# Kernel optimization log

Measured on AMD Instinct MI355X. Metric: run time of the kernel, lower is better.

## Reference

```python
import jax, jax.numpy as jnp
import numpy as np

IN_F = 4096
OUT_F = 11008
P8 = 128
P6 = 256
P4 = IN_F - P8 - P6  # 3712


def setup_inputs() -> dict:
    key = jax.random.key(0)
    k1, k2, k3, k4 = jax.random.split(key, 4)
    x = jax.random.normal(k1, (32, 8, IN_F), dtype=jnp.float32)
    W = jax.random.normal(k2, (OUT_F, IN_F), dtype=jnp.float32) * 0.02
    bias = jax.random.normal(k3, (OUT_F,), dtype=jnp.float32) * 0.01
    # channel permutation: first P4 channels -> 4-bit, next P6 -> 6-bit, last P8 -> 8-bit outliers
    reorder_index = jax.random.permutation(k4, IN_F).astype(jnp.int32)
    return {"x": x, "W": W, "bias": bias, "reorder_index": reorder_index}


def _quant(v, bits):
    # symmetric per-row quantization (per-token for acts, per-out-channel for weights)
    qmax = float(2 ** (bits - 1) - 1)
    s = jnp.max(jnp.abs(v), axis=-1, keepdims=True) / qmax
    s = jnp.where(s == 0, jnp.ones_like(s), s)
    q = jnp.round(jnp.clip(v / s, -qmax, qmax))
    return q, s


def reference(x, W, bias, reorder_index):
    bsz, q_len, F = x.shape
    xr = x.reshape(bsz * q_len, F)[:, reorder_index]  # reorder_quantize_x gather
    Wr = W[:, reorder_index]                          # reorder_quantize_w4 gather
    y = jnp.zeros((bsz * q_len, W.shape[0]), dtype=x.dtype)
    start = 0
    for bits, n in ((4, P4), (6, P6), (8, P8)):
        qa, sa = _quant(xr[:, start:start + n], bits)      # [T,n], [T,1]
        qb, sb = _quant(Wr[:, start:start + n], bits)      # [O,n], [O,1]
        # dequantized partial matmul: (qa @ qb.T) * sa * sb.T
        y = y + jnp.einsum('tn,on->to', qa, qb) * (sa * sb.T)
        start += n
    y = y + bias
    return y.reshape(bsz, q_len, -1)
```

## Files before the change

kernel.cpp:

```cpp
#include <hip/hip_runtime.h>
#include <stdint.h>

#define T_ROWS 256
#define KF 4096
#define OF 11008
#define WROW 2240

typedef int   v4i __attribute__((ext_vector_type(4)));
typedef float v4f __attribute__((ext_vector_type(4)));
typedef unsigned int u32;

typedef const __attribute__((address_space(1))) uint8_t* gptr_t;
typedef __attribute__((address_space(3))) uint8_t* lptr_t;

__global__ __launch_bounds__(256) void perm_k(const int* __restrict__ idx,
                                              int* __restrict__ src_of) {
    __shared__ uint8_t g[KF];
    __shared__ int cnt[3][256];
    __shared__ int exc[3][256];
    const int t = threadIdx.x;
    for (int i = 0; i < 16; ++i) {
        int p = t * 16 + i;
        int seg = p < 3712 ? 0 : (p < 3968 ? 1 : 2);
        g[idx[p]] = (uint8_t)seg;
    }
    __syncthreads();
    int c0 = 0, c1 = 0, c2 = 0;
    for (int i = 0; i < 16; ++i) {
        int s = g[t * 16 + i];
        c0 += (s == 0); c1 += (s == 1); c2 += (s == 2);
    }
    cnt[0][t] = c0; cnt[1][t] = c1; cnt[2][t] = c2;
    __syncthreads();
    if (t < 192) {
        int s = t >> 6, l = t & 63;
        int run = 0;
        for (int j = 0; j < 4; ++j) {
            int x = cnt[s][j * 64 + l];
            int inc = x;
#pragma unroll
            for (int off = 1; off < 64; off <<= 1) {
                int y = __shfl_up(inc, off);
                if (l >= off) inc += y;
            }
            exc[s][j * 64 + l] = run + inc - x;
            run += __shfl(inc, 63);
        }
    }
    __syncthreads();
    int off0 = exc[0][t], off1 = 3712 + exc[1][t], off2 = 3968 + exc[2][t];
    for (int i = 0; i < 16; ++i) {
        int c = t * 16 + i;
        int s = g[c];
        int d = (s == 0) ? off0++ : (s == 1) ? off1++ : off2++;
        src_of[d] = c;
    }
}

__global__ __launch_bounds__(256) void quant_k(const float* __restrict__ x,
                                               const float* __restrict__ W,
                                               const int* __restrict__ src_of,
                                               int8_t* __restrict__ qX,
                                               uint8_t* __restrict__ qWp,
                                               float* __restrict__ sX,
                                               float* __restrict__ sW,
                                               int* __restrict__ S0X) {
    __shared__ float rowbuf[KF];
    __shared__ float lmax[256];
    __shared__ float sm[3];
    __shared__ int isum[256];
    const int b = blockIdx.x;
    const int t = threadIdx.x;
    const int w = t >> 6, lane = t & 63;
    const bool isX = b < T_ROWS;
    const int r = isX ? b : b - T_ROWS;
    const float* row = (isX ? x : W) + (size_t)r * KF;

#pragma unroll
    for (int j = 0; j < 4; ++j) {
        const uint8_t* src = (const uint8_t*)(row + j * 1024 + t * 4);
        __builtin_amdgcn_global_load_lds((gptr_t)src, (lptr_t)&rowbuf[j * 1024 + w * 256], 16, 0, 0);
    }

    const int seg = t < 232 ? 0 : (t < 248 ? 1 : 2);
    const float qmax = seg == 0 ? 7.f : (seg == 1 ? 31.f : 127.f);
    int c[16];
#pragma unroll
    for (int i = 0; i < 4; ++i) {
        v4i ci = *(const v4i*)&src_of[t * 16 + i * 4];
        c[i*4+0] = ci[0]; c[i*4+1] = ci[1]; c[i*4+2] = ci[2]; c[i*4+3] = ci[3];
    }
    __syncthreads();

    float v[16];
    float mx = 0.f;
#pragma unroll
    for (int i = 0; i < 16; ++i) { v[i] = rowbuf[c[i]]; mx = fmaxf(mx, fabsf(v[i])); }
    lmax[t] = mx;
    __syncthreads();
    if (w == 0) {
        float m = fmaxf(fmaxf(lmax[lane], lmax[lane + 64]), lmax[lane + 128]);
        if (lane < 40) m = fmaxf(m, lmax[lane + 192]);
#pragma unroll
        for (int off = 32; off; off >>= 1) m = fmaxf(m, __shfl_xor(m, off));
        if (lane == 0) sm[0] = m;
    } else if (w == 1) {
        float m = lane < 16 ? lmax[232 + lane] : 0.f;
#pragma unroll
        for (int off = 8; off; off >>= 1) m = fmaxf(m, __shfl_xor(m, off));
        if (lane == 0) sm[1] = m;
    } else if (w == 2) {
        float m = lane < 8 ? lmax[248 + lane] : 0.f;
#pragma unroll
        for (int off = 4; off; off >>= 1) m = fmaxf(m, __shfl_xor(m, off));
        if (lane == 0) sm[2] = m;
    }
    __syncthreads();
    float s = sm[seg] / qmax;
    if (s == 0.f) s = 1.f;
    if (t == 0 || t == 232 || t == 248)
        (isX ? sX : sW)[seg * (isX ? T_ROWS : OF) + r] = s;

    int q[16];
#pragma unroll
    for (int i = 0; i < 16; ++i)
        q[i] = (int)rintf(fminf(fmaxf(v[i] / s, -qmax), qmax));

    if (isX) {
        int ss = 0;
        union { int8_t bb[16]; v4i vv; } u;
#pragma unroll
        for (int i = 0; i < 16; ++i) { u.bb[i] = (int8_t)q[i]; ss += q[i]; }
        isum[t] = (seg == 0) ? ss : 0;
        *(v4i*)(qX + (size_t)r * KF + t * 16) = u.vv;
        __syncthreads();
        if (w == 0) {
            int v2 = isum[lane] + isum[lane + 64] + isum[lane + 128] + isum[lane + 192];
#pragma unroll
            for (int off = 32; off; off >>= 1) v2 += __shfl_xor(v2, off);
            if (lane == 0) S0X[r] = v2;
        }
    } else {
        uint8_t* wrow = qWp + (size_t)r * WROW;
        if (seg == 0) {
            u32 pk[2] = {0, 0};
#pragma unroll
            for (int j = 0; j < 8; ++j) {
                u32 byte = (u32)(q[2*j] + 8) | ((u32)(q[2*j+1] + 8) << 4);
                pk[j >> 2] |= byte << ((j & 3) * 8);
            }
            *(u32*)(wrow + t * 8) = pk[0];
            *(u32*)(wrow + t * 8 + 4) = pk[1];
        } else {
            union { int8_t bb[16]; v4i vv; } u;
#pragma unroll
            for (int i = 0; i < 16; ++i) u.bb[i] = (int8_t)q[i];
            const int off = (seg == 1) ? 1856 + (t - 232) * 16 : 2112 + (t - 248) * 16;
            *(v4i*)(wrow + off) = u.vv;
        }
    }
}

__global__ __launch_bounds__(256, 2)
void gemm_k(const int8_t* __restrict__ qX, const uint8_t* __restrict__ qWp,
            const float* __restrict__ sX, const float* __restrict__ sW,
            const int* __restrict__ S0X,
            const float* __restrict__ bias, float* __restrict__ out) {
    __shared__ __align__(16) int8_t lA[3][128 * 128];
    __shared__ __align__(16) int8_t lB[2][64 * 128];

    const int bid = blockIdx.x;
    const int swz = (bid & 7) * 43 + (bid >> 3);
    const int mb = swz & 1;
    const int nb = swz >> 1;
    const int row0 = mb * 128;
    const int col0 = nb * 64;
    const int tid = threadIdx.x;
    const int lane = tid & 63;
    const int w = tid >> 6;
    const int lr = lane >> 3, lc = lane & 7;
    const int brow = tid >> 2;
    const int bch  = tid & 3;

    v4i iacc[2][4];
    v4f facc[2][4];
#pragma unroll
    for (int m = 0; m < 2; ++m)
#pragma unroll
        for (int n = 0; n < 4; ++n) {
            iacc[m][n][0]=0; iacc[m][n][1]=0; iacc[m][n][2]=0; iacc[m][n][3]=0;
            facc[m][n][0]=0.f; facc[m][n][1]=0.f; facc[m][n][2]=0.f; facc[m][n][3]=0.f;
        }

    auto stageA = [&](int slot, int step) {
        const int k0 = step * 128;
        const int sc = (lc ^ lr) << 4;
#pragma unroll
        for (int j = 0; j < 4; ++j) {
            const int row = j * 32 + w * 8;
            const uint8_t* src = (const uint8_t*)qX + (size_t)(row0 + row + lr) * KF + k0 + sc;
            __builtin_amdgcn_global_load_lds((gptr_t)src, (lptr_t)&lA[slot][row * 128], 16, 0, 0);
        }
    };

    auto loadB = [&](v4i (&rs)[2], int step) {
        const uint8_t* rb = qWp + (size_t)(col0 + brow) * WROW;
        if (step <= 28) {
            rs[0] = *(const v4i*)(rb + step * 64 + bch * 16);
        } else {
            const int off = step * 128 - 1856;
            rs[0] = *(const v4i*)(rb + off + bch * 32);
            rs[1] = *(const v4i*)(rb + off + bch * 32 + 16);
        }
    };

    auto writeB = [&](v4i (&rs)[2], int step) {
        int8_t* dst = &lB[step & 1][0];
        const int swr = brow & 7;
        v4i w0, w1;
        if (step <= 28) {
#pragma unroll
            for (int qq = 0; qq < 4; ++qq) {
                u32 wd = ((u32)((const int*)&rs[0])[qq]);
                u32 lo = wd & 0x0F0F0F0Fu;
                u32 hi = (wd >> 4) & 0x0F0F0F0Fu;
                u32 e0 = __builtin_amdgcn_perm(hi, lo, 0x05010400u);
                u32 e1 = __builtin_amdgcn_perm(hi, lo, 0x07030602u);
                if (qq < 2) { w0[2*qq] = (int)e0; w0[2*qq+1] = (int)e1; }
                else        { w1[2*(qq-2)] = (int)e0; w1[2*(qq-2)+1] = (int)e1; }
            }
        } else {
            w0 = rs[0]; w1 = rs[1];
        }
        *(v4i*)(dst + brow * 128 + ((2 * bch)     ^ swr) * 16) = w0;
        *(v4i*)(dst + brow * 128 + ((2 * bch + 1) ^ swr) * 16) = w1;
    };

    auto flush = [&](int seg) {
#pragma unroll
        for (int m = 0; m < 2; ++m) {
            float sa[4]; int s0[4];
#pragma unroll
            for (int rr = 0; rr < 4; ++rr) {
                const int rg = row0 + w * 32 + m * 16 + ((lane >> 4) << 2) + rr;
                sa[rr] = sX[seg * T_ROWS + rg];
                s0[rr] = (seg == 0) ? S0X[rg] : 0;
            }
#pragma unroll
            for (int n = 0; n < 4; ++n) {
                const float sb = sW[seg * OF + col0 + n * 16 + (lane & 15)];
#pragma unroll
                for (int rr = 0; rr < 4; ++rr) {
                    const int v = iacc[m][n][rr] - 8 * s0[rr];
                    facc[m][n][rr] += (float)v * (sa[rr] * sb);
                    iacc[m][n][rr] = 0;
                }
            }
        }
    };

    auto body = [&](int t, v4i (&rsLoad)[2], v4i (&rsWrite)[2]) {
        __builtin_amdgcn_s_barrier();
        v4i a[2][2], bfr[4][2];
        const int kg = lane >> 4;
        const int8_t* pa = &lA[t % 3][0];
        const int8_t* pb = &lB[t & 1][0];
#pragma unroll
        for (int m = 0; m < 2; ++m) {
            const int row = w * 32 + m * 16 + (lane & 15);
#pragma unroll
            for (int kk = 0; kk < 2; ++kk) {
                const int ch = (kk * 4 + kg) ^ (row & 7);
                a[m][kk] = *(const v4i*)(pa + row * 128 + ch * 16);
            }
        }
#pragma unroll
        for (int n = 0; n < 4; ++n) {
            const int row = n * 16 + (lane & 15);
#pragma unroll
            for (int kk = 0; kk < 2; ++kk) {
                const int ch = (kk * 4 + kg) ^ (row & 7);
                bfr[n][kk] = *(const v4i*)(pb + row * 128 + ch * 16);
            }
        }
        asm volatile("s_waitcnt lgkmcnt(0)" ::: "memory");
        __builtin_amdgcn_sched_barrier(0);
#pragma unroll
        for (int kk = 0; kk < 2; ++kk)
#pragma unroll
            for (int m = 0; m < 2; ++m)
#pragma unroll
                for (int n = 0; n < 4; ++n)
                    iacc[m][n] = __builtin_amdgcn_mfma_i32_16x16x64_i8(a[m][kk], bfr[n][kk], iacc[m][n], 0, 0, 0);
        if (t == 28) flush(0);
        else if (t == 30) flush(1);
        if (t + 2 < 32) {
            stageA((t + 2) % 3, t + 2);
            loadB(rsLoad, t + 2);
            if (t + 2 <= 28) asm volatile("s_waitcnt vmcnt(5)" ::: "memory");
            else             asm volatile("s_waitcnt vmcnt(6)" ::: "memory");
        } else {
            asm volatile("s_waitcnt vmcnt(0)" ::: "memory");
        }
        if (t + 1 < 32) {
            writeB(rsWrite, t + 1);
            asm volatile("s_waitcnt lgkmcnt(0)" ::: "memory");
        }
    };

    v4i rsA_[2], rsB_[2];
    stageA(0, 0);
    loadB(rsA_, 0);
    asm volatile("s_waitcnt vmcnt(0)" ::: "memory");
    writeB(rsA_, 0);
    stageA(1, 1);
    loadB(rsB_, 1);
    asm volatile("s_waitcnt lgkmcnt(0)" ::: "memory");

    for (int tt = 0; tt < 32; tt += 2) {
        body(tt,     rsA_, rsB_);
        body(tt + 1, rsB_, rsA_);
    }
    flush(2);

#pragma unroll
    for (int m = 0; m < 2; ++m)
#pragma unroll
        for (int n = 0; n < 4; ++n) {
            const int colg = col0 + n * 16 + (lane & 15);
            const float bv = bias[colg];
#pragma unroll
            for (int rr = 0; rr < 4; ++rr) {
                const int rowg = row0 + w * 32 + m * 16 + ((lane >> 4) << 2) + rr;
                out[(size_t)rowg * OF + colg] = facc[m][n][rr] + bv;
            }
        }
}

extern "C" void kernel_launch(void* const* d_in, const int* in_sizes, int n_in,
                              void* d_out, int out_size, void* d_ws, size_t ws_size,
                              hipStream_t stream) {
    const float* x    = (const float*)d_in[0];
    const float* W    = (const float*)d_in[1];
    const float* bias = (const float*)d_in[2];
    const int*   ridx = (const int*)d_in[3];
    float* out = (float*)d_out;

    uint8_t* ws = (uint8_t*)d_ws;
    int8_t*  qX  = (int8_t*)ws;
    uint8_t* qWp = ws + 1048576;
    float*   sX  = (float*)(ws + 25706496);
    float*   sW  = (float*)(ws + 25709568);
    int* src_of  = (int*)(ws + 25841664);
    int* S0X     = (int*)(ws + 25858048);

    perm_k<<<1, 256, 0, stream>>>(ridx, src_of);
    quant_k<<<T_ROWS + OF, 256, 0, stream>>>(x, W, src_of, qX, qWp, sX, sW, S0X);
    gemm_k<<<344, 256, 0, stream>>>(qX, qWp, sX, sW, S0X, bias, out);
}
```

Measured before the change: 83.28 us.

## Load weight fragments directly from global into registers, dropping LDS staging for B

Weight packing is reordered so that each lane's MFMA B fragment can be read with contiguous 16-byte global loads. The GEMM then loads B straight into registers one step ahead and unpacks the 4-bit values in registers, removing the B shared-memory buffer, its writes and the associated LDS waits. This frees LDS and cuts LDS traffic. In exchange, B rows are no longer shared through LDS, so the waves that use the same columns each read them from global, raising global load count and register pressure. The vmcnt wait counts were retuned by hand for the new load mix.

```diff
diff --git a/kernel.cpp b/kernel.cpp
--- a/kernel.cpp
+++ b/kernel.cpp
@@ -149,8 +149,9 @@
                 u32 byte = (u32)(q[2*j] + 8) | ((u32)(q[2*j+1] + 8) << 4);
                 pk[j >> 2] |= byte << ((j & 3) * 8);
             }
-            *(u32*)(wrow + t * 8) = pk[0];
-            *(u32*)(wrow + t * 8 + 4) = pk[1];
+            const int b0 = ((t >> 3) * 64) + ((t & 3) * 16) + (((t >> 2) & 1) * 8);
+            *(u32*)(wrow + b0) = pk[0];
+            *(u32*)(wrow + b0 + 4) = pk[1];
         } else {
             union { int8_t bb[16]; v4i vv; } u;
 #pragma unroll
@@ -159,6 +160,17 @@
             *(v4i*)(wrow + off) = u.vv;
         }
     }
+}
+
+__device__ __forceinline__ v4i unpack8(u32 d0, u32 d1) {
+    v4i r;
+    u32 lo0 = d0 & 0x0F0F0F0Fu, hi0 = (d0 >> 4) & 0x0F0F0F0Fu;
+    u32 lo1 = d1 & 0x0F0F0F0Fu, hi1 = (d1 >> 4) & 0x0F0F0F0Fu;
+    r[0] = (int)__builtin_amdgcn_perm(hi0, lo0, 0x05010400u);
+    r[1] = (int)__builtin_amdgcn_perm(hi0, lo0, 0x07030602u);
+    r[2] = (int)__builtin_amdgcn_perm(hi1, lo1, 0x05010400u);
+    r[3] = (int)__builtin_amdgcn_perm(hi1, lo1, 0x07030602u);
+    return r;
 }
 
 __global__ __launch_bounds__(256, 2)
@@ -167,20 +179,17 @@
             const int* __restrict__ S0X,
             const float* __restrict__ bias, float* __restrict__ out) {
     __shared__ __align__(16) int8_t lA[3][128 * 128];
-    __shared__ __align__(16) int8_t lB[2][64 * 128];
 
     const int bid = blockIdx.x;
     const int swz = (bid & 7) * 43 + (bid >> 3);
-    const int mb = swz & 1;
-    const int nb = swz >> 1;
-    const int row0 = mb * 128;
-    const int col0 = nb * 64;
+    const int row0 = (swz & 1) * 128;
+    const int col0 = (swz >> 1) * 64;
     const int tid = threadIdx.x;
     const int lane = tid & 63;
     const int w = tid >> 6;
     const int lr = lane >> 3, lc = lane & 7;
-    const int brow = tid >> 2;
-    const int bch  = tid & 3;
+    const int kg = lane >> 4;
+    const int cr = lane & 15;
 
     v4i iacc[2][4];
     v4f facc[2][4];
@@ -192,48 +201,35 @@
             facc[m][n][0]=0.f; facc[m][n][1]=0.f; facc[m][n][2]=0.f; facc[m][n][3]=0.f;
         }
 
+    const uint8_t* rowB[4];
+#pragma unroll
+    for (int n = 0; n < 4; ++n)
+        rowB[n] = qWp + (size_t)(col0 + n * 16 + cr) * WROW;
+
     auto stageA = [&](int slot, int step) {
         const int k0 = step * 128;
         const int sc = (lc ^ lr) << 4;
 #pragma unroll
         for (int j = 0; j < 4; ++j) {
-            const int row = j * 32 + w * 8;
-            const uint8_t* src = (const uint8_t*)qX + (size_t)(row0 + row + lr) * KF + k0 + sc;
-            __builtin_amdgcn_global_load_lds((gptr_t)src, (lptr_t)&lA[slot][row * 128], 16, 0, 0);
+            const int arow = j * 32 + w * 8;
+            const uint8_t* src = (const uint8_t*)qX + (size_t)(row0 + arow + lr) * KF + k0 + sc;
+            __builtin_amdgcn_global_load_lds((gptr_t)src, (lptr_t)&lA[slot][arow * 128], 16, 0, 0);
         }
     };
 
-    auto loadB = [&](v4i (&rs)[2], int step) {
-        const uint8_t* rb = qWp + (size_t)(col0 + brow) * WROW;
+    auto loadB = [&](v4i (&rb)[8], int step) {
         if (step <= 28) {
-            rs[0] = *(const v4i*)(rb + step * 64 + bch * 16);
+#pragma unroll
+            for (int n = 0; n < 4; ++n)
+                rb[n] = *(const v4i*)(rowB[n] + step * 64 + kg * 16);
         } else {
-            const int off = step * 128 - 1856;
-            rs[0] = *(const v4i*)(rb + off + bch * 32);
-            rs[1] = *(const v4i*)(rb + off + bch * 32 + 16);
-        }
-    };
-
-    auto writeB = [&](v4i (&rs)[2], int step) {
-        int8_t* dst = &lB[step & 1][0];
-        const int swr = brow & 7;
-        v4i w0, w1;
-        if (step <= 28) {
-#pragma unroll
-            for (int qq = 0; qq < 4; ++qq) {
-                u32 wd = ((u32)((const int*)&rs[0])[qq]);
-                u32 lo = wd & 0x0F0F0F0Fu;
-                u32 hi = (wd >> 4) & 0x0F0F0F0Fu;
-                u32 e0 = __builtin_amdgcn_perm(hi, lo, 0x05010400u);
-                u32 e1 = __builtin_amdgcn_perm(hi, lo, 0x07030602u);
-                if (qq < 2) { w0[2*qq] = (int)e0; w0[2*qq+1] = (int)e1; }
-                else        { w1[2*(qq-2)] = (int)e0; w1[2*(qq-2)+1] = (int)e1; }
-            }
-        } else {
-            w0 = rs[0]; w1 = rs[1];
-        }
-        *(v4i*)(dst + brow * 128 + ((2 * bch)     ^ swr) * 16) = w0;
-        *(v4i*)(dst + brow * 128 + ((2 * bch + 1) ^ swr) * 16) = w1;
+            const int off = 1856 + step * 128 - 3712 + kg * 16;
+#pragma unroll
+            for (int n = 0; n < 4; ++n) {
+                rb[n]     = *(const v4i*)(rowB[n] + off);
+                rb[n + 4] = *(const v4i*)(rowB[n] + off + 64);
+            }
+        }
     };
 
     auto flush = [&](int seg) {
@@ -259,67 +255,55 @@
         }
     };
 
-    auto body = [&](int t, v4i (&rsLoad)[2], v4i (&rsWrite)[2]) {
+    auto body = [&](int t, v4i (&rbCur)[8], v4i (&rbNext)[8]) {
         __builtin_amdgcn_s_barrier();
-        v4i a[2][2], bfr[4][2];
-        const int kg = lane >> 4;
+        v4i a[2][2];
         const int8_t* pa = &lA[t % 3][0];
-        const int8_t* pb = &lB[t & 1][0];
 #pragma unroll
         for (int m = 0; m < 2; ++m) {
-            const int row = w * 32 + m * 16 + (lane & 15);
+            const int arow = w * 32 + m * 16 + cr;
 #pragma unroll
             for (int kk = 0; kk < 2; ++kk) {
-                const int ch = (kk * 4 + kg) ^ (row & 7);
-                a[m][kk] = *(const v4i*)(pa + row * 128 + ch * 16);
-            }
-        }
-#pragma unroll
-        for (int n = 0; n < 4; ++n) {
-            const int row = n * 16 + (lane & 15);
-#pragma unroll
-            for (int kk = 0; kk < 2; ++kk) {
-                const int ch = (kk * 4 + kg) ^ (row & 7);
-                bfr[n][kk] = *(const v4i*)(pb + row * 128 + ch * 16);
-            }
-        }
-        asm volatile("s_waitcnt lgkmcnt(0)" ::: "memory");
-        __builtin_amdgcn_sched_barrier(0);
+                const int ch = (kk * 4 + kg) ^ (arow & 7);
+                a[m][kk] = *(const v4i*)(pa + arow * 128 + ch * 16);
+            }
+        }
+        if (t + 2 < 32) stageA((t + 2) % 3, t + 2);
+        if (t + 1 < 32) loadB(rbNext, t + 1);
+        v4i bf[4][2];
+        if (t <= 28) {
+#pragma unroll
+            for (int n = 0; n < 4; ++n) {
+                bf[n][0] = unpack8((u32)rbCur[n][0], (u32)rbCur[n][1]);
+                bf[n][1] = unpack8((u32)rbCur[n][2], (u32)rbCur[n][3]);
+            }
+        } else {
+#pragma unroll
+            for (int n = 0; n < 4; ++n) { bf[n][0] = rbCur[n]; bf[n][1] = rbCur[n + 4]; }
+        }
 #pragma unroll
         for (int kk = 0; kk < 2; ++kk)
 #pragma unroll
             for (int m = 0; m < 2; ++m)
 #pragma unroll
                 for (int n = 0; n < 4; ++n)
-                    iacc[m][n] = __builtin_amdgcn_mfma_i32_16x16x64_i8(a[m][kk], bfr[n][kk], iacc[m][n], 0, 0, 0);
+                    iacc[m][n] = __builtin_amdgcn_mfma_i32_16x16x64_i8(a[m][kk], bf[n][kk], iacc[m][n], 0, 0, 0);
         if (t == 28) flush(0);
         else if (t == 30) flush(1);
-        if (t + 2 < 32) {
-            stageA((t + 2) % 3, t + 2);
-            loadB(rsLoad, t + 2);
-            if (t + 2 <= 28) asm volatile("s_waitcnt vmcnt(5)" ::: "memory");
-            else             asm volatile("s_waitcnt vmcnt(6)" ::: "memory");
-        } else {
-            asm volatile("s_waitcnt vmcnt(0)" ::: "memory");
-        }
-        if (t + 1 < 32) {
-            writeB(rsWrite, t + 1);
-            asm volatile("s_waitcnt lgkmcnt(0)" ::: "memory");
-        }
+        if (t <= 27)      asm volatile("s_waitcnt vmcnt(8)"  ::: "memory");
+        else if (t <= 29) asm volatile("s_waitcnt vmcnt(12)" ::: "memory");
+        else if (t == 30) asm volatile("s_waitcnt vmcnt(8)"  ::: "memory");
     };
 
-    v4i rsA_[2], rsB_[2];
+    v4i rbA_[8], rbB_[8];
     stageA(0, 0);
-    loadB(rsA_, 0);
-    asm volatile("s_waitcnt vmcnt(0)" ::: "memory");
-    writeB(rsA_, 0);
     stageA(1, 1);
-    loadB(rsB_, 1);
-    asm volatile("s_waitcnt lgkmcnt(0)" ::: "memory");
+    loadB(rbA_, 0);
+    asm volatile("s_waitcnt vmcnt(8)" ::: "memory");
 
     for (int tt = 0; tt < 32; tt += 2) {
-        body(tt,     rsA_, rsB_);
-        body(tt + 1, rsB_, rsA_);
+        body(tt,     rbA_, rbB_);
+        body(tt + 1, rbB_, rbA_);
     }
     flush(2);
 
```

New measurement: 107.3 us. 28.9% more time.
